# Kernel tuning notes

Measured on AMD Instinct MI355X. Metric: run time of the kernel, lower is better.

The kernel has to match this reference:

```python
import jax, jax.numpy as jnp
import numpy as np

B, S, DIM, NH = 4, 2048, 2048, 16
HD = DIM // NH  # 128


def setup_inputs() -> dict:
    key = jax.random.key(0)
    ks = jax.random.split(key, 6)
    x = jax.random.normal(ks[0], (B, S, DIM), dtype=jnp.float32)
    wq = jax.random.normal(ks[1], (DIM, DIM), dtype=jnp.float32) * (DIM ** -0.5)
    wk = jax.random.normal(ks[2], (DIM, DIM), dtype=jnp.float32) * (DIM ** -0.5)
    wv = jax.random.normal(ks[3], (DIM, DIM), dtype=jnp.float32) * (DIM ** -0.5)
    wo = jax.random.normal(ks[4], (DIM, DIM), dtype=jnp.float32) * (DIM ** -0.5)
    # RoPE frequencies: theta^{-2i/hd}, angle = pos * freq
    inv_freq = 1.0 / (10000.0 ** (np.arange(0, HD, 2, dtype=np.float32) / HD))  # [HD/2]
    angles = np.arange(S, dtype=np.float32)[:, None] * inv_freq[None, :]  # [S, HD/2]
    freqs_cos = jnp.asarray(np.cos(angles))
    freqs_sin = jnp.asarray(np.sin(angles))
    # causal mask, additive [S, S]
    mask = jnp.where(jnp.tril(jnp.ones((S, S), dtype=bool)), 0.0, -jnp.inf).astype(jnp.float32)
    return {"x": x, "wq": wq, "wk": wk, "wv": wv, "wo": wo,
            "freqs_cos": freqs_cos, "freqs_sin": freqs_sin, "mask": mask,
            "start_pos": 0}


def _apply_rotary(xq, xk, cos, sin):
    # xq, xk: [B, S, H, HD]; cos/sin: [S, HD/2]
    def rot(t):
        tr = t.reshape(*t.shape[:-1], -1, 2)  # [B,S,H,HD/2,2]
        a, b = tr[..., 0], tr[..., 1]
        c = cos[None, :, None, :]
        s = sin[None, :, None, :]
        # complex multiply (a+ib)(c+is)
        out = jnp.stack([a * c - b * s, a * s + b * c], axis=-1)
        return out.reshape(t.shape)
    return rot(xq), rot(xk)


def reference(x, wq, wk, wv, wo, freqs_cos, freqs_sin, mask, start_pos):
    bsz, seqlen, _ = x.shape
    # nn.Linear: y = x @ W^T
    xq = (x @ wq.T).reshape(bsz, seqlen, NH, HD)
    xk = (x @ wk.T).reshape(bsz, seqlen, NH, HD)
    xv = (x @ wv.T).reshape(bsz, seqlen, NH, HD)
    xq, xk = _apply_rotary(xq, xk, freqs_cos, freqs_sin)
    # attention, heads to axis 1
    scores = jnp.einsum('bqhd,bkhd->bhqk', xq, xk) / jnp.sqrt(jnp.float32(HD))
    scores = scores + mask[None, None, :, :]
    probs = jax.nn.softmax(scores.astype(jnp.float32), axis=-1).astype(xq.dtype)
    out = jnp.einsum('bhqk,bkhd->bqhd', probs, xv).reshape(bsz, seqlen, -1)
    return out @ wo.T
```

## Files before the change

### kernel.cpp

```cpp
#include <hip/hip_runtime.h>

typedef __attribute__((ext_vector_type(8))) __bf16 bf16x8;
typedef __attribute__((ext_vector_type(4))) float f32x4;
typedef __attribute__((ext_vector_type(16))) float f32x16;
typedef __attribute__((ext_vector_type(8))) unsigned short u16x8;
typedef __attribute__((ext_vector_type(2))) unsigned uint2v;

#define LOG2E 1.44269504088896340736f

__device__ __forceinline__ unsigned short f2bf(float f){
  union { float f; unsigned u; } v; v.f = f;
  unsigned r = v.u + 0x7FFFu + ((v.u >> 16) & 1u);
  return (unsigned short)(r >> 16);
}
__device__ __forceinline__ float bf2f(unsigned short u){
  union { unsigned u; float f; } v; v.u = ((unsigned)u) << 16;
  return v.f;
}

typedef const unsigned __attribute__((address_space(1)))* gas_ptr;
typedef unsigned __attribute__((address_space(3)))* las_ptr;

__device__ __forceinline__ void gload_lds16(const void* g, void* l){
  __builtin_amdgcn_global_load_lds((gas_ptr)g, (las_ptr)l, 16, 0, 0);
}

__device__ __forceinline__ unsigned cvtpk(float lo, float hi){
  unsigned r;
  asm("v_cvt_pk_bf16_f32 %0, %1, %2" : "=v"(r) : "v"(lo), "v"(hi));
  return r;
}
__device__ __forceinline__ void swap32(unsigned &a, unsigned &b){
  uint2v r = __builtin_amdgcn_permlane32_swap(a, b, false, false);
  a = r[0]; b = r[1];
}
__device__ __forceinline__ float xsum32(float v){
  union { float f; unsigned u; } a; a.f = v;
  uint2v r = __builtin_amdgcn_permlane32_swap(a.u, a.u, false, false);
  union { unsigned u; float f; } x, y; x.u = r[0]; y.u = r[1];
  return x.f + y.f;
}

__global__ __launch_bounds__(256) void cvt_f32_bf16(const float* __restrict__ in,
                                                    unsigned short* __restrict__ out){
  size_t i = ((size_t)blockIdx.x * 256 + threadIdx.x) * 4;
  float4 vv = *(const float4*)(in + i);
  ushort4 o;
  o.x = f2bf(vv.x); o.y = f2bf(vv.y); o.z = f2bf(vv.z); o.w = f2bf(vv.w);
  *(ushort4*)(out + i) = o;
}
__global__ __launch_bounds__(256) void cvt_w4(const float* __restrict__ w0, const float* __restrict__ w1,
                                              const float* __restrict__ w2, const float* __restrict__ w3,
                                              unsigned short* o0, unsigned short* o1,
                                              unsigned short* o2, unsigned short* o3){
  const float* in = blockIdx.y == 0 ? w0 : blockIdx.y == 1 ? w1 : blockIdx.y == 2 ? w2 : w3;
  unsigned short* out = blockIdx.y == 0 ? o0 : blockIdx.y == 1 ? o1 : blockIdx.y == 2 ? o2 : o3;
  size_t i = ((size_t)blockIdx.x * 256 + threadIdx.x) * 4;
  float4 vv = *(const float4*)(in + i);
  ushort4 o;
  o.x = f2bf(vv.x); o.y = f2bf(vv.y); o.z = f2bf(vv.z); o.w = f2bf(vv.w);
  *(ushort4*)(out + i) = o;
}

#define BUF(op, half, par) (LDS + (((op) * 2 + (half)) * 2 + (par)) * 16384)

#define STAGE(op, gbase, half, par, kt) do {                                   \
  _Pragma("unroll")                                                            \
  for (int c_ = 0; c_ < 2; ++c_){                                              \
    int slot_ = c_ * 512 + w * 64 + l;                                         \
    int row_ = slot_ >> 3, colb_ = slot_ & 7;                                  \
    gload_lds16((const char*)((gbase) + (size_t)((half) * 128 + row_) * K +    \
                              (size_t)(kt) * 64 + ((colb_ ^ (row_ & 7)) * 8)), \
                BUF(op, half, par) + c_ * 8192 + w * 1024);                    \
  } } while (0)

#define RD_A(buf) do {                                                         \
  const char* Ab_ = (buf);                                                     \
  _Pragma("unroll")                                                            \
  for (int i_ = 0; i_ < 4; ++i_){                                              \
    int row_ = wm * 64 + i_ * 16 + lq;                                         \
    _Pragma("unroll")                                                          \
    for (int ks_ = 0; ks_ < 2; ++ks_)                                          \
      aA[i_][ks_] = *(const bf16x8*)(Ab_ + row_ * 128 +                        \
                                     (((ks_ * 4 + lg) ^ (row_ & 7)) * 16));    \
  } } while (0)

#define RD_B(buf, arr) do {                                                    \
  const char* Bb_ = (buf);                                                     \
  _Pragma("unroll")                                                            \
  for (int j_ = 0; j_ < 2; ++j_){                                              \
    int row_ = wn * 32 + j_ * 16 + lq;                                         \
    _Pragma("unroll")                                                          \
    for (int ks_ = 0; ks_ < 2; ++ks_)                                          \
      arr[j_][ks_] = *(const bf16x8*)(Bb_ + row_ * 128 +                       \
                                      (((ks_ * 4 + lg) ^ (row_ & 7)) * 16));   \
  } } while (0)

#define DO_MFMA(mh, nh, arr, tail) do {                                        \
  __builtin_amdgcn_s_barrier();                                                \
  asm volatile("s_waitcnt lgkmcnt(0)");                                        \
  __builtin_amdgcn_s_setprio(1);                                               \
  _Pragma("unroll")                                                            \
  for (int i_ = 0; i_ < 4; ++i_)                                               \
    _Pragma("unroll")                                                          \
    for (int j_ = 0; j_ < 2; ++j_)                                             \
      _Pragma("unroll")                                                        \
      for (int ks_ = 0; ks_ < 2; ++ks_)                                        \
        acc[(mh) * 4 + i_][(nh) * 2 + j_] = __builtin_amdgcn_mfma_f32_16x16x32_bf16( \
            aA[i_][ks_], arr[j_][ks_], acc[(mh) * 4 + i_][(nh) * 2 + j_], 0, 0, 0); \
  __builtin_amdgcn_s_setprio(0);                                               \
  tail;                                                                        \
  __builtin_amdgcn_s_barrier();                                                \
} while (0)

template<bool OUT_BF16, bool ROPE>
__global__ __launch_bounds__(512, 2) void gemm256(const unsigned short* __restrict__ A,
                                                  const unsigned short* __restrict__ B,
                                                  void* __restrict__ Cv,
                                                  int M, int N, int K,
                                                  const float* __restrict__ fc,
                                                  const float* __restrict__ fs){
  __shared__ char LDS[131072];
  const int tid = threadIdx.x;
  const int l = tid & 63, w = tid >> 6;
  const int lq = l & 15, lg = l >> 4;
  const int wm = w >> 2, wn = w & 3;

  const int nwg = gridDim.x, cpx = nwg >> 3;
  const int orig = blockIdx.x;
  const int sw = (orig & 7) * cpx + (orig >> 3);
  const int nbc = N >> 8;
  const int br = sw / nbc, bc = sw % nbc;

  f32x4 acc[8][4] = {};
  bf16x8 aA[4][2], bB0[2][2], bB1[2][2];
  const unsigned short* Ag = A + (size_t)br * 256 * K;
  const unsigned short* Bg = B + (size_t)bc * 256 * K;
  const int NT = K >> 6;

  STAGE(0, Ag, 0, 0, 0); STAGE(1, Bg, 0, 0, 0);
  STAGE(0, Ag, 1, 0, 0); STAGE(1, Bg, 1, 0, 0);
  STAGE(1, Bg, 0, 1, 1); STAGE(0, Ag, 0, 1, 1);
  asm volatile("s_waitcnt vmcnt(4)" ::: "memory");
  __builtin_amdgcn_s_barrier();

  for (int t = 0; t < NT; ++t){
    const int par = t & 1, parn = par ^ 1;
    RD_A(BUF(0, 0, par));
    RD_B(BUF(1, 0, par), bB0);
    if (t + 1 < NT) STAGE(0, Ag, 1, parn, t + 1);
    DO_MFMA(0, 0, bB0, (void)0);
    RD_B(BUF(1, 1, par), bB1);
    if (t + 1 < NT) STAGE(1, Bg, 1, parn, t + 1);
    DO_MFMA(0, 1, bB1, (void)0);
    RD_A(BUF(0, 1, par));
    if (t + 2 < NT) STAGE(0, Ag, 0, par, t + 2);
    DO_MFMA(1, 0, bB0, (void)0);
    if (t + 2 < NT) STAGE(1, Bg, 0, par, t + 2);
    DO_MFMA(1, 1, bB1, asm volatile("s_waitcnt vmcnt(4)" ::: "memory"));
  }

#pragma unroll
  for (int i = 0; i < 8; ++i){
    int grow = br * 256 + (i >> 2) * 128 + wm * 64 + (i & 3) * 16 + lg * 4;
#pragma unroll
    for (int j = 0; j < 4; ++j){
      int gcol = bc * 256 + (j >> 1) * 128 + wn * 32 + (j & 1) * 16 + lq;
#pragma unroll
      for (int r = 0; r < 4; ++r){
        float v = acc[i][j][r];
        if (ROPE){
          int s = (grow + r) & 2047;
          int i0 = (gcol & 127) >> 1;
          float cc = fc[s * 64 + i0], sn = fs[s * 64 + i0];
          float part = __shfl_xor(v, 1, 64);
          v = (lq & 1) ? __builtin_fmaf(part, sn, v * cc)
                       : __builtin_fmaf(-part, sn, v * cc);
        }
        if (OUT_BF16)
          ((unsigned short*)Cv)[(size_t)(grow + r) * N + gcol] = f2bf(v);
        else
          ((float*)Cv)[(size_t)(grow + r) * N + gcol] = v;
      }
    }
  }
}

__global__ __launch_bounds__(512, 2) void attn_fwd(const unsigned short* __restrict__ Q,
                                                   const unsigned short* __restrict__ K,
                                                   const unsigned short* __restrict__ V,
                                                   unsigned short* __restrict__ O){
  __shared__ unsigned short SMEM[2 * 64 * 128 + 2 * 128 * 64];
  unsigned short* Ks = SMEM;
  unsigned short* Vt = SMEM + 16384;

  const int tid = threadIdx.x;
  const int l = tid & 63, wid = tid >> 6;
  const int lq = l & 31, hi = l >> 5;
  const int bh = blockIdx.x & 63;
  const int tsel = blockIdx.x >> 8;
  const int kidx = (blockIdx.x >> 6) & 3;
  const int qt = tsel ? kidx : 7 - kidx;
  const int b = bh >> 4, h = bh & 15;
  const int qw = qt * 256 + wid * 32;
  const float c2 = 0.12751743f;

  const unsigned short* qptr = Q + ((size_t)(b * 2048 + qw + lq)) * 2048 + (size_t)h * 128;
  bf16x8 qf[8];
#pragma unroll
  for (int ks = 0; ks < 8; ++ks){
    u16x8 qr = *(const u16x8*)(qptr + ks * 16 + hi * 8);
    union { unsigned u[4]; bf16x8 v; } qq;
#pragma unroll
    for (int e = 0; e < 4; ++e)
      qq.u[e] = cvtpk(bf2f(qr[2 * e]) * c2, bf2f(qr[2 * e + 1]) * c2);
    qf[ks] = qq.v;
  }

  f32x16 oacc[4];
#pragma unroll
  for (int i = 0; i < 4; ++i)
#pragma unroll
    for (int j = 0; j < 16; ++j) oacc[i][j] = 0.f;
  float lrow = 0.f;

  const int dblk = tid >> 5, kvp = tid & 31;
  const size_t hb = (size_t)b * 2048 * 2048 + (size_t)h * 128;
  u16x8 r0, r1;

  {
    const size_t kvb = hb;
#pragma unroll
    for (int c = 0; c < 2; ++c){
      int off = c * 8192 + tid * 16;
      int row = off >> 8, colb = off & 255;
      gload_lds16((const char*)(K + kvb + (size_t)row * 2048) + (colb ^ ((row & 15) << 4)),
                  (char*)Ks + c * 8192 + (tid >> 6) * 1024 + (tid & 63) * 16);
    }
    const unsigned short* vp = V + kvb + (size_t)(2 * kvp) * 2048 + dblk * 8;
    r0 = *(const u16x8*)vp; r1 = *(const u16x8*)(vp + 2048);
    asm volatile("s_waitcnt vmcnt(0)" ::: "memory");
#pragma unroll
    for (int j = 0; j < 8; ++j){
      int d = dblk * 8 + j;
      unsigned val = (unsigned)r0[j] | ((unsigned)r1[j] << 16);
      *(unsigned*)((char*)Vt + d * 128 + ((4 * kvp) ^ ((d & 7) << 4))) = val;
    }
  }
  __syncthreads();

  const int nkt = 4 * qt + 4;
  for (int kt = 0; kt < nkt; ++kt){
    const int cur = kt & 1, nxt = cur ^ 1;
    const bool pref = (kt + 1 < nkt);
    char* KsC = (char*)(Ks + cur * 8192);
    char* VtC = (char*)(Vt + cur * 8192);

    if (pref){
      const size_t kvb = hb + (size_t)((kt + 1) * 64) * 2048;
      char* KsN = (char*)(Ks + nxt * 8192);
#pragma unroll
      for (int c = 0; c < 2; ++c){
        int off = c * 8192 + tid * 16;
        int row = off >> 8, colb = off & 255;
        gload_lds16((const char*)(K + kvb + (size_t)row * 2048) + (colb ^ ((row & 15) << 4)),
                    KsN + c * 8192 + (tid >> 6) * 1024 + (tid & 63) * 16);
      }
      const unsigned short* vp = V + kvb + (size_t)(2 * kvp) * 2048 + dblk * 8;
      r0 = *(const u16x8*)vp; r1 = *(const u16x8*)(vp + 2048);
    }

    if (!(kt * 64 > qw + 31)){
      f32x16 sacc[2];
#pragma unroll
      for (int sub = 0; sub < 2; ++sub){
#pragma unroll
        for (int j = 0; j < 16; ++j) sacc[sub][j] = 0.f;
        const int row = sub * 32 + lq;
        const int swz = (row & 15) << 4;
#pragma unroll
        for (int ks = 0; ks < 8; ++ks){
          bf16x8 kf = *(const bf16x8*)(KsC + row * 256 + ((ks * 32 + hi * 16) ^ swz));
          sacc[sub] = __builtin_amdgcn_mfma_f32_32x32x16_bf16(kf, qf[ks], sacc[sub], 0, 0, 0);
        }
      }

      float s[32];
#pragma unroll
      for (int sub = 0; sub < 2; ++sub)
#pragma unroll
        for (int r = 0; r < 16; ++r) s[sub * 16 + r] = sacc[sub][r];

      if (kt * 64 + 63 > qw){
        const int qg = qw + lq;
#pragma unroll
        for (int sub = 0; sub < 2; ++sub)
#pragma unroll
          for (int r = 0; r < 16; ++r){
            int kvg = kt * 64 + sub * 32 + (r & 3) + 8 * (r >> 2) + 4 * hi;
            if (kvg > qg) s[sub * 16 + r] = -3.0e38f;
          }
      }

      float p[32];
#pragma unroll
      for (int i = 0; i < 32; ++i)
        p[i] = __builtin_amdgcn_exp2f(s[i]);
      float sm[32];
#pragma unroll
      for (int i = 0; i < 32; ++i) sm[i] = p[i];
#pragma unroll
      for (int st = 1; st < 32; st <<= 1)
#pragma unroll
        for (int i = 0; i < 32; i += 2 * st) sm[i] += sm[i + st];
      lrow += xsum32(sm[0]);

      unsigned wv[16];
#pragma unroll
      for (int i = 0; i < 16; ++i) wv[i] = cvtpk(p[2 * i], p[2 * i + 1]);
      swap32(wv[0], wv[2]);   swap32(wv[1], wv[3]);
      swap32(wv[4], wv[6]);   swap32(wv[5], wv[7]);
      swap32(wv[8], wv[10]);  swap32(wv[9], wv[11]);
      swap32(wv[12], wv[14]); swap32(wv[13], wv[15]);

#pragma unroll
      for (int c = 0; c < 4; ++c){
        union { unsigned u[4]; bf16x8 v; } pu;
        pu.u[0] = wv[c * 4 + 0]; pu.u[1] = wv[c * 4 + 1];
        pu.u[2] = wv[c * 4 + 2]; pu.u[3] = wv[c * 4 + 3];
#pragma unroll
        for (int db = 0; db < 4; ++db){
          const int d = db * 32 + lq;
          bf16x8 vf = *(const bf16x8*)(VtC + d * 128 + ((c * 32 + hi * 16) ^ ((d & 7) << 4)));
          oacc[db] = __builtin_amdgcn_mfma_f32_32x32x16_bf16(vf, pu.v, oacc[db], 0, 0, 0);
        }
      }
    }

    if (pref){
      asm volatile("s_waitcnt vmcnt(0)" ::: "memory");
      char* VtN = (char*)(Vt + nxt * 8192);
#pragma unroll
      for (int j = 0; j < 8; ++j){
        int d = dblk * 8 + j;
        unsigned val = (unsigned)r0[j] | ((unsigned)r1[j] << 16);
        *(unsigned*)(VtN + d * 128 + ((4 * kvp) ^ ((d & 7) << 4))) = val;
      }
    }
    __syncthreads();
  }

  float inv = 1.0f / lrow;
  char* lb = (char*)SMEM + wid * 8192;
#pragma unroll
  for (int db = 0; db < 4; ++db)
#pragma unroll
    for (int r = 0; r < 16; r += 2){
      int d = db * 32 + (r & 3) + 8 * (r >> 2) + 4 * hi;
      unsigned val = (unsigned)f2bf(oacc[db][r] * inv) |
                     ((unsigned)f2bf(oacc[db][r + 1] * inv) << 16);
      *(unsigned*)(lb + lq * 256 + ((2 * d) ^ ((lq & 7) << 4))) = val;
    }
  __syncthreads();
#pragma unroll
  for (int i = 0; i < 8; ++i){
    int rowq = i * 4 + (l >> 4);
    u16x8 vv = *(const u16x8*)(lb + rowq * 256 + (((l & 15) * 16) ^ ((rowq & 7) << 4)));
    *(u16x8*)(O + ((size_t)(b * 2048 + qw + rowq)) * 2048 + (size_t)h * 128 + (l & 15) * 8) = vv;
  }
}

extern "C" void kernel_launch(void* const* d_in, const int* in_sizes, int n_in,
                              void* d_out, int out_size, void* d_ws, size_t ws_size,
                              hipStream_t stream){
  const float* x  = (const float*)d_in[0];
  const float* wq = (const float*)d_in[1];
  const float* wk = (const float*)d_in[2];
  const float* wv = (const float*)d_in[3];
  const float* wo = (const float*)d_in[4];
  const float* fc = (const float*)d_in[5];
  const float* fs = (const float*)d_in[6];
  float* out = (float*)d_out;
  (void)in_sizes; (void)n_in; (void)out_size; (void)ws_size;

  const size_t XN = (size_t)8192 * 2048;
  const size_t WN = (size_t)2048 * 2048;

  unsigned short* xb  = (unsigned short*)d_ws;
  unsigned short* wqb = xb + XN;
  unsigned short* wkb = wqb + WN;
  unsigned short* wvb = wkb + WN;
  unsigned short* wob = wvb + WN;
  unsigned short* q   = wob + WN;
  unsigned short* k   = q + XN;
  unsigned short* v   = k + XN;
  unsigned short* att = xb;

  cvt_f32_bf16<<<dim3((unsigned)(XN / 1024)), 256, 0, stream>>>(x, xb);
  cvt_w4<<<dim3((unsigned)(WN / 1024), 4), 256, 0, stream>>>(wq, wk, wv, wo, wqb, wkb, wvb, wob);

  gemm256<true, true ><<<dim3(256), 512, 0, stream>>>(xb, wqb, q, 8192, 2048, 2048, fc, fs);
  gemm256<true, true ><<<dim3(256), 512, 0, stream>>>(xb, wkb, k, 8192, 2048, 2048, fc, fs);
  gemm256<true, false><<<dim3(256), 512, 0, stream>>>(xb, wvb, v, 8192, 2048, 2048, nullptr, nullptr);

  attn_fwd<<<dim3(512), 512, 0, stream>>>(q, k, v, att);

  gemm256<false, false><<<dim3(256), 512, 0, stream>>>(att, wob, out, 8192, 2048, 2048, nullptr, nullptr);
}
```

Baseline: 387.4 us.

## Fuse QKV projections into one launch and switch GEMM to 32x32x16 MFMA

The three Q/K/V projection GEMMs become a single 768-block launch, with each block picking its weight matrix and output buffer from its tile index, and RoPE is applied only to the Q and K tiles. The GEMM inner loop now uses 32x32x16 bf16 MFMA instructions with 16-element accumulators instead of 16x16x32, and the LDS fragment reads are remapped to match. Bf16 output stores pair neighbouring lanes through a shuffle so each store writes 32 bits. This aims to cut launch tail effects, raise MFMA efficiency and reduce store transactions, at the cost of different register pressure and a new fragment layout whose correctness has to hold.

```diff
diff --git a/kernel.cpp b/kernel.cpp
--- a/kernel.cpp
+++ b/kernel.cpp
@@ -5,8 +5,6 @@
 typedef __attribute__((ext_vector_type(16))) float f32x16;
 typedef __attribute__((ext_vector_type(8))) unsigned short u16x8;
 typedef __attribute__((ext_vector_type(2))) unsigned uint2v;
-
-#define LOG2E 1.44269504088896340736f
 
 __device__ __forceinline__ unsigned short f2bf(float f){
   union { float f; unsigned u; } v; v.f = f;
@@ -77,65 +75,70 @@
 #define RD_A(buf) do {                                                         \
   const char* Ab_ = (buf);                                                     \
   _Pragma("unroll")                                                            \
-  for (int i_ = 0; i_ < 4; ++i_){                                              \
-    int row_ = wm * 64 + i_ * 16 + lq;                                         \
+  for (int m_ = 0; m_ < 2; ++m_){                                              \
+    int row_ = wm * 64 + m_ * 32 + lq;                                         \
     _Pragma("unroll")                                                          \
-    for (int ks_ = 0; ks_ < 2; ++ks_)                                          \
-      aA[i_][ks_] = *(const bf16x8*)(Ab_ + row_ * 128 +                        \
-                                     (((ks_ * 4 + lg) ^ (row_ & 7)) * 16));    \
+    for (int k_ = 0; k_ < 4; ++k_)                                             \
+      aA[m_][k_] = *(const bf16x8*)(Ab_ + row_ * 128 +                         \
+                                    (((k_ * 2 + hi) ^ (row_ & 7)) * 16));      \
   } } while (0)
 
 #define RD_B(buf, arr) do {                                                    \
   const char* Bb_ = (buf);                                                     \
+  int row_ = wn * 32 + lq;                                                     \
   _Pragma("unroll")                                                            \
-  for (int j_ = 0; j_ < 2; ++j_){                                              \
-    int row_ = wn * 32 + j_ * 16 + lq;                                         \
-    _Pragma("unroll")                                                          \
-    for (int ks_ = 0; ks_ < 2; ++ks_)                                          \
-      arr[j_][ks_] = *(const bf16x8*)(Bb_ + row_ * 128 +                       \
-                                      (((ks_ * 4 + lg) ^ (row_ & 7)) * 16));   \
-  } } while (0)
+  for (int k_ = 0; k_ < 4; ++k_)                                               \
+    arr[k_] = *(const bf16x8*)(Bb_ + row_ * 128 +                              \
+                               (((k_ * 2 + hi) ^ (row_ & 7)) * 16));           \
+  } while (0)
 
 #define DO_MFMA(mh, nh, arr, tail) do {                                        \
   __builtin_amdgcn_s_barrier();                                                \
   asm volatile("s_waitcnt lgkmcnt(0)");                                        \
   __builtin_amdgcn_s_setprio(1);                                               \
   _Pragma("unroll")                                                            \
-  for (int i_ = 0; i_ < 4; ++i_)                                               \
+  for (int m_ = 0; m_ < 2; ++m_)                                               \
     _Pragma("unroll")                                                          \
-    for (int j_ = 0; j_ < 2; ++j_)                                             \
-      _Pragma("unroll")                                                        \
-      for (int ks_ = 0; ks_ < 2; ++ks_)                                        \
-        acc[(mh) * 4 + i_][(nh) * 2 + j_] = __builtin_amdgcn_mfma_f32_16x16x32_bf16( \
-            aA[i_][ks_], arr[j_][ks_], acc[(mh) * 4 + i_][(nh) * 2 + j_], 0, 0, 0); \
+    for (int k_ = 0; k_ < 4; ++k_)                                             \
+      acc[(mh) * 2 + m_][nh] = __builtin_amdgcn_mfma_f32_32x32x16_bf16(        \
+          aA[m_][k_], arr[k_], acc[(mh) * 2 + m_][nh], 0, 0, 0);               \
   __builtin_amdgcn_s_setprio(0);                                               \
   tail;                                                                        \
   __builtin_amdgcn_s_barrier();                                                \
 } while (0)
 
-template<bool OUT_BF16, bool ROPE>
+template<bool QKV, bool OUT_BF16>
 __global__ __launch_bounds__(512, 2) void gemm256(const unsigned short* __restrict__ A,
-                                                  const unsigned short* __restrict__ B,
-                                                  void* __restrict__ Cv,
+                                                  const unsigned short* __restrict__ B0,
+                                                  const unsigned short* __restrict__ B1,
+                                                  const unsigned short* __restrict__ B2,
+                                                  void* __restrict__ C0,
+                                                  void* __restrict__ C1,
+                                                  void* __restrict__ C2,
                                                   int M, int N, int K,
                                                   const float* __restrict__ fc,
                                                   const float* __restrict__ fs){
   __shared__ char LDS[131072];
   const int tid = threadIdx.x;
   const int l = tid & 63, w = tid >> 6;
-  const int lq = l & 15, lg = l >> 4;
+  const int lq = l & 31, hi = l >> 5;
   const int wm = w >> 2, wn = w & 3;
 
-  const int nwg = gridDim.x, cpx = nwg >> 3;
+  const int cpx = gridDim.x >> 3;
   const int orig = blockIdx.x;
   const int sw = (orig & 7) * cpx + (orig >> 3);
-  const int nbc = N >> 8;
-  const int br = sw / nbc, bc = sw % nbc;
-
-  f32x4 acc[8][4] = {};
-  bf16x8 aA[4][2], bB0[2][2], bB1[2][2];
+  const int nbc = QKV ? 24 : (N >> 8);
+  const int br = sw / nbc, bcg = sw % nbc;
+  const int wsel = QKV ? (bcg >> 3) : 0;
+  const int bc = QKV ? (bcg & 7) : bcg;
+  const unsigned short* Bg = (QKV ? (wsel == 0 ? B0 : wsel == 1 ? B1 : B2) : B0)
+                             + (size_t)bc * 256 * K;
+  void* Cv = QKV ? (wsel == 0 ? C0 : wsel == 1 ? C1 : C2) : C0;
+  const bool rope = QKV && (wsel < 2);
+
+  f32x16 acc[4][2] = {};
+  bf16x8 aA[2][4], bB0[4], bB1[4];
   const unsigned short* Ag = A + (size_t)br * 256 * K;
-  const unsigned short* Bg = B + (size_t)bc * 256 * K;
   const int NT = K >> 6;
 
   STAGE(0, Ag, 0, 0, 0); STAGE(1, Bg, 0, 0, 0);
@@ -161,26 +164,31 @@
   }
 
 #pragma unroll
-  for (int i = 0; i < 8; ++i){
-    int grow = br * 256 + (i >> 2) * 128 + wm * 64 + (i & 3) * 16 + lg * 4;
-#pragma unroll
-    for (int j = 0; j < 4; ++j){
-      int gcol = bc * 256 + (j >> 1) * 128 + wn * 32 + (j & 1) * 16 + lq;
-#pragma unroll
-      for (int r = 0; r < 4; ++r){
-        float v = acc[i][j][r];
-        if (ROPE){
-          int s = (grow + r) & 2047;
+  for (int i = 0; i < 4; ++i){
+    int rowb = br * 256 + (i >> 1) * 128 + wm * 64 + (i & 1) * 32;
+#pragma unroll
+    for (int nh = 0; nh < 2; ++nh){
+      int gcol = bc * 256 + nh * 128 + wn * 32 + lq;
+#pragma unroll
+      for (int r = 0; r < 16; ++r){
+        int grow = rowb + (r & 3) + 8 * (r >> 2) + 4 * hi;
+        float v = acc[i][nh][r];
+        if (rope){
+          int s = grow & 2047;
           int i0 = (gcol & 127) >> 1;
           float cc = fc[s * 64 + i0], sn = fs[s * 64 + i0];
           float part = __shfl_xor(v, 1, 64);
           v = (lq & 1) ? __builtin_fmaf(part, sn, v * cc)
                        : __builtin_fmaf(-part, sn, v * cc);
         }
-        if (OUT_BF16)
-          ((unsigned short*)Cv)[(size_t)(grow + r) * N + gcol] = f2bf(v);
-        else
-          ((float*)Cv)[(size_t)(grow + r) * N + gcol] = v;
+        if (OUT_BF16){
+          unsigned wb = f2bf(v);
+          unsigned pn = __shfl_xor((int)wb, 1, 64);
+          if (!(lq & 1))
+            *(unsigned*)((unsigned short*)Cv + (size_t)grow * N + gcol) = wb | (pn << 16);
+        } else {
+          ((float*)Cv)[(size_t)grow * N + gcol] = v;
+        }
       }
     }
   }
@@ -399,11 +407,12 @@
   cvt_f32_bf16<<<dim3((unsigned)(XN / 1024)), 256, 0, stream>>>(x, xb);
   cvt_w4<<<dim3((unsigned)(WN / 1024), 4), 256, 0, stream>>>(wq, wk, wv, wo, wqb, wkb, wvb, wob);
 
-  gemm256<true, true ><<<dim3(256), 512, 0, stream>>>(xb, wqb, q, 8192, 2048, 2048, fc, fs);
-  gemm256<true, true ><<<dim3(256), 512, 0, stream>>>(xb, wkb, k, 8192, 2048, 2048, fc, fs);
-  gemm256<true, false><<<dim3(256), 512, 0, stream>>>(xb, wvb, v, 8192, 2048, 2048, nullptr, nullptr);
+  gemm256<true, true><<<dim3(768), 512, 0, stream>>>(xb, wqb, wkb, wvb,
+                                                     q, k, v, 8192, 2048, 2048, fc, fs);
 
   attn_fwd<<<dim3(512), 512, 0, stream>>>(q, k, v, att);
 
-  gemm256<false, false><<<dim3(256), 512, 0, stream>>>(att, wob, out, 8192, 2048, 2048, nullptr, nullptr);
-}
+  gemm256<false, false><<<dim3(256), 512, 0, stream>>>(att, wob, wob, wob,
+                                                       out, out, out, 8192, 2048, 2048,
+                                                       nullptr, nullptr);
+}
```

Result: slower. 494.2 us (+27.6%).
